# Performance work log

Measured on AMD Instinct MI355X. Metric: run time of the kernel, lower is better.

## Reference

```python
import jax, jax.numpy as jnp
import numpy as np

B, H, W, C = 16, 32, 32, 512
L, CT = 77, 512
NH, HD = 8, 64
G = 32          # GroupNorm groups
EPS = 1e-6      # flax GroupNorm default epsilon
NEG = -1e10


def group_norm(x, scale, bias):
    # flax GroupNorm on [b, n, c]: stats over (n, channels-within-group) per (b, group)
    b, n, c = x.shape
    xg = x.reshape(b, n, G, c // G)
    mu = xg.mean(axis=(1, 3), keepdims=True)
    var = xg.var(axis=(1, 3), keepdims=True)
    xg = (xg - mu) * jax.lax.rsqrt(var + EPS)
    return xg.reshape(b, n, c) * scale + bias


def setup_inputs() -> dict:
    key = jax.random.key(0)
    ks = jax.random.split(key, 8)
    w = lambda k, shape: jax.random.normal(k, shape, jnp.float32) * 0.02
    return {
        "inputs": jax.random.normal(ks[0], (B, H, W, C), jnp.float32),
        "text_enc": jax.random.normal(ks[1], (B, L, CT), jnp.float32),
        "text_mask": jnp.ones((B, L), jnp.int32),
        "gn_q_scale": jnp.ones((C,), jnp.float32),
        "gn_q_bias": jnp.zeros((C,), jnp.float32),
        "gn_kv_scale": jnp.ones((C,), jnp.float32),
        "gn_kv_bias": jnp.zeros((C,), jnp.float32),
        "gn_t_scale": jnp.ones((CT,), jnp.float32),
        "gn_t_bias": jnp.zeros((CT,), jnp.float32),
        "Wq": w(ks[2], (C, NH, HD)),
        "Wk_self": w(ks[3], (C, NH, HD)),
        "Wv_self": w(ks[4], (C, NH, HD)),
        "Wk_cross": w(ks[5], (CT, NH, HD)),
        "Wv_cross": w(ks[6], (CT, NH, HD)),
        "Wout": w(ks[7], (NH, HD, C)),
    }


def reference(inputs, text_enc, text_mask,
              gn_q_scale, gn_q_bias, gn_kv_scale, gn_kv_bias,
              gn_t_scale, gn_t_bias,
              Wq, Wk_self, Wv_self, Wk_cross, Wv_cross, Wout):
    b, h, w, c = inputs.shape
    n = h * w
    x = inputs.reshape(b, n, c)

    x_q = group_norm(x, gn_q_scale, gn_q_bias)
    x_kv = group_norm(x, gn_kv_scale, gn_kv_bias)
    t = group_norm(text_enc, gn_t_scale, gn_t_bias)

    # q/k/v projections; fused: KV = concat(self-KV from image, cross-KV from text)
    scale = jnp.asarray(1.0 / np.sqrt(HD), inputs.dtype)
    q = jnp.einsum('bqc,chd->bqhd', x_q, Wq) * scale  # scale_attn_logits
    k = jnp.concatenate([jnp.einsum('bkc,chd->bkhd', x_kv, Wk_self),
                         jnp.einsum('blc,chd->blhd', t, Wk_cross)], axis=1)
    v = jnp.concatenate([jnp.einsum('bkc,chd->bkhd', x_kv, Wv_self),
                         jnp.einsum('blc,chd->blhd', t, Wv_cross)], axis=1)

    # make_attention_mask(ones[b,n], concat(ones[b,n], text_mask)) -> [b,1,n,n+l];
    # query mask is all ones so only the KV mask matters.
    kv_mask = jnp.concatenate(
        [jnp.ones((b, n), jnp.bool_), text_mask > 0], axis=1)  # [b, n+l]

    logits = jnp.einsum('bqhd,bkhd->bhqk', q, k)  # [b, nh, n, n+l]
    logits = jnp.where(kv_mask[:, None, None, :], logits, jnp.asarray(NEG, logits.dtype))
    probs = jax.nn.softmax(logits, axis=-1)
    attn = jnp.einsum('bhqk,bkhd->bqhd', probs, v)
    out = jnp.einsum('bqhd,hdc->bqc', attn, Wout)
    return out.reshape(b, h, w, c) + inputs
```

## Files before the change

kernel.cpp:

```cpp
#include <hip/hip_runtime.h>
#include <hip/hip_bf16.h>

typedef __hip_bfloat16 bf16;
typedef __attribute__((ext_vector_type(8))) short short8;
typedef __attribute__((ext_vector_type(4))) float f32x4;
typedef __attribute__((ext_vector_type(16))) float f32x16;
#define MFMA16(a, b, c) __builtin_amdgcn_mfma_f32_16x16x32_bf16(a, b, c, 0, 0, 0)
#define MFMA32(a, b, c) __builtin_amdgcn_mfma_f32_32x32x16_bf16(a, b, c, 0, 0, 0)

#define BB   16
#define CCH  512
#define NN   1024
#define LLT  77
#define LPAD 128
#define NHH  8
#define HDD  64
#define GGN  32
#define NKV  1101
#define KVP  1152
#define QSC  0.18033688f

__device__ __forceinline__ unsigned short f2bu(float f){
  bf16 h = __float2bfloat16(f);
  return *reinterpret_cast<unsigned short*>(&h);
}

__device__ __forceinline__ unsigned pk2(float lo, float hi){
  unsigned r;
  asm("v_cvt_pk_bf16_f32 %0, %1, %2" : "=v"(r) : "v"(lo), "v"(hi));
  return r;
}

__device__ __forceinline__ float fexp2(float x){
  float r;
  asm("v_exp_f32 %0, %1" : "=v"(r) : "v"(x));
  return r;
}

__device__ __forceinline__ void pl32swap(unsigned &a, unsigned &b){
  asm("v_permlane32_swap_b32 %0, %1" : "+v"(a), "+v"(b));
}

__device__ __forceinline__ void gload16(const bf16* g, bf16* l){
  __builtin_amdgcn_global_load_lds(
      (const __attribute__((address_space(1))) unsigned int*)g,
      (__attribute__((address_space(3))) unsigned int*)l,
      16, 0, 0);
}

__global__ __launch_bounds__(256) void gn_norm_kernel(
    const float* __restrict__ x, const float* __restrict__ t,
    const float* __restrict__ gqs, const float* __restrict__ gqb,
    const float* __restrict__ gks, const float* __restrict__ gkb,
    const float* __restrict__ gts, const float* __restrict__ gtb,
    const float* __restrict__ W0, const float* __restrict__ W1,
    const float* __restrict__ W2, const float* __restrict__ W3,
    const float* __restrict__ W4, const float* __restrict__ W5,
    bf16* __restrict__ Wt,
    bf16* __restrict__ Xq, bf16* __restrict__ Xkv, bf16* __restrict__ Tn)
{
  __shared__ float sh1[256], sh2[256], mr[2];
  __shared__ alignas(16) float Ws[64][68];
  const int tid = threadIdx.x;
  const int bid = blockIdx.x;

  if (bid < 512){
    const int b = bid >> 5, g = bid & 31;
    const float* xb = x + (size_t)b * NN * CCH + g * 16;
    float s = 0.f, s2 = 0.f;
    for (int i = tid; i < 4096; i += 256){
      const int n = i >> 2, cq = (i & 3) * 4;
      float4 v = *(const float4*)(xb + (size_t)n * CCH + cq);
      s  += v.x + v.y + v.z + v.w;
      s2 += v.x * v.x + v.y * v.y + v.z * v.z + v.w * v.w;
    }
    sh1[tid] = s; sh2[tid] = s2;
    __syncthreads();
    for (int off = 128; off > 0; off >>= 1){
      if (tid < off){ sh1[tid] += sh1[tid + off]; sh2[tid] += sh2[tid + off]; }
      __syncthreads();
    }
    if (tid == 0){
      const float inv = 1.f / 16384.f;
      const float m = sh1[0] * inv;
      mr[0] = m;
      mr[1] = rsqrtf(sh2[0] * inv - m * m + 1e-6f);
    }
    __syncthreads();
    const float m = mr[0], r = mr[1];
    const int ch0 = g * 16;
    for (int i = tid; i < 4096; i += 256){
      const int n = i >> 2, cq = (i & 3) * 4;
      const int ch = ch0 + cq;
      float4 v  = *(const float4*)(xb + (size_t)n * CCH + cq);
      float4 sq = *(const float4*)(gqs + ch), bq = *(const float4*)(gqb + ch);
      float4 sk = *(const float4*)(gks + ch), bk = *(const float4*)(gkb + ch);
      const float n0 = (v.x - m) * r, n1 = (v.y - m) * r;
      const float n2 = (v.z - m) * r, n3 = (v.w - m) * r;
      uint2 oq, ok;
      oq.x = pk2((n0 * sq.x + bq.x) * QSC, (n1 * sq.y + bq.y) * QSC);
      oq.y = pk2((n2 * sq.z + bq.z) * QSC, (n3 * sq.w + bq.w) * QSC);
      ok.x = pk2(n0 * sk.x + bk.x, n1 * sk.y + bk.y);
      ok.y = pk2(n2 * sk.z + bk.z, n3 * sk.w + bk.w);
      const size_t off = ((size_t)b * NN + n) * CCH + ch;
      *(uint2*)(Xq  + off) = oq;
      *(uint2*)(Xkv + off) = ok;
    }
  } else if (bid < 1024){
    const int b = (bid - 512) >> 5, g = (bid - 512) & 31;
    const float* tb = t + (size_t)b * LLT * CCH + g * 16;
    float s = 0.f, s2 = 0.f;
    for (int i = tid; i < 308; i += 256){
      const int l = i >> 2, cq = (i & 3) * 4;
      float4 v = *(const float4*)(tb + (size_t)l * CCH + cq);
      s  += v.x + v.y + v.z + v.w;
      s2 += v.x * v.x + v.y * v.y + v.z * v.z + v.w * v.w;
    }
    sh1[tid] = s; sh2[tid] = s2;
    __syncthreads();
    for (int off = 128; off > 0; off >>= 1){
      if (tid < off){ sh1[tid] += sh1[tid + off]; sh2[tid] += sh2[tid + off]; }
      __syncthreads();
    }
    if (tid == 0){
      const float inv = 1.f / (float)(LLT * 16);
      const float m = sh1[0] * inv;
      mr[0] = m;
      mr[1] = rsqrtf(sh2[0] * inv - m * m + 1e-6f);
    }
    __syncthreads();
    const float m = mr[0], r = mr[1];
    const int ch0 = g * 16;
    for (int i = tid; i < 512; i += 256){
      const int l = i >> 2, cq = (i & 3) * 4;
      const int ch = ch0 + cq;
      uint2 o;
      if (l < LLT){
        float4 v  = *(const float4*)(tb + (size_t)l * CCH + cq);
        float4 sv = *(const float4*)(gts + ch), bv = *(const float4*)(gtb + ch);
        o.x = pk2((v.x - m) * r * sv.x + bv.x, (v.y - m) * r * sv.y + bv.y);
        o.y = pk2((v.z - m) * r * sv.z + bv.z, (v.w - m) * r * sv.w + bv.w);
      } else {
        o.x = 0u; o.y = 0u;
      }
      *(uint2*)(Tn + ((size_t)b * LPAD + l) * CCH + ch) = o;
    }
  } else {
    const int i = bid - 1024;
    const int wsel = i >> 6;
    const int rem  = i & 63;
    const int n0 = (rem & 7) * 64, k0 = (rem >> 3) * 64;
    const float* W = wsel == 0 ? W0 : wsel == 1 ? W1 : wsel == 2 ? W2 :
                     wsel == 3 ? W3 : wsel == 4 ? W4 : W5;
    bf16* dst = Wt + (size_t)wsel * CCH * CCH;

    const int rr = tid >> 2, c = (tid & 3) * 16;
    const float* src = W + (size_t)(k0 + rr) * CCH + n0 + c;
    *(float4*)&Ws[rr][c]      = *(const float4*)(src);
    *(float4*)&Ws[rr][c + 4]  = *(const float4*)(src + 4);
    *(float4*)&Ws[rr][c + 8]  = *(const float4*)(src + 8);
    *(float4*)&Ws[rr][c + 12] = *(const float4*)(src + 12);
    __syncthreads();

    const int nr = tid >> 2, kc = (tid & 3) * 16;
    uint4 o0, o1;
    o0.x = pk2(Ws[kc + 0][nr],  Ws[kc + 1][nr]);
    o0.y = pk2(Ws[kc + 2][nr],  Ws[kc + 3][nr]);
    o0.z = pk2(Ws[kc + 4][nr],  Ws[kc + 5][nr]);
    o0.w = pk2(Ws[kc + 6][nr],  Ws[kc + 7][nr]);
    o1.x = pk2(Ws[kc + 8][nr],  Ws[kc + 9][nr]);
    o1.y = pk2(Ws[kc + 10][nr], Ws[kc + 11][nr]);
    o1.z = pk2(Ws[kc + 12][nr], Ws[kc + 13][nr]);
    o1.w = pk2(Ws[kc + 14][nr], Ws[kc + 15][nr]);
    bf16* d = dst + (size_t)(n0 + nr) * CCH + k0 + kc;
    *(uint4*)d = o0;
    *(uint4*)(d + 8) = o1;
  }
}

__global__ __launch_bounds__(256) void proj_all_mfma(
    const bf16* __restrict__ Xq, const bf16* __restrict__ Xkv,
    const bf16* __restrict__ Tn, const bf16* __restrict__ Wt,
    bf16* __restrict__ Qo, bf16* __restrict__ Ko, bf16* __restrict__ Vo)
{
  __shared__ alignas(16) char SHRAW[65536];
  const int tid  = threadIdx.x;
  const int wave = tid >> 6, lane = tid & 63;
  const int l16 = lane & 15, quad = lane >> 4;
  const int bx = blockIdx.x;

  if (bx < 1536){
    bf16 (*T)[4][64][64] = reinterpret_cast<bf16(*)[4][64][64]>(SHRAW);
    const int wr = wave >> 1, wc = wave & 1;
    const int ct = bx >> 7;
    const int rt = bx & 127;
    const int mat = ct >> 2;
    const int cm0 = (ct & 3) * 128;
    const int b  = rt >> 3;
    const int n0 = (rt & 7) * 128;

    const bf16* A  = (mat == 0) ? Xq : Xkv;
    const bf16* Bw = Wt + (size_t)mat * CCH * CCH + (size_t)cm0 * CCH;

    f32x4 acc[4][4];
    #pragma unroll
    for (int rf = 0; rf < 4; rf++)
      #pragma unroll
      for (int cf = 0; cf < 4; cf++) acc[rf][cf] = (f32x4){0.f,0.f,0.f,0.f};

    const int lrow = lane >> 3, lcol = (lane & 7) * 8;
    const bf16* srcbase = (wave < 2)
        ? A  + ((size_t)b * NN + n0 + wave * 64) * CCH
        : Bw + (size_t)((wave - 2) * 64) * CCH;

    #pragma unroll
    for (int c = 0; c < 8; c++)
      gload16(srcbase + (size_t)(c * 8 + lrow) * CCH + lcol, &T[0][wave][c * 8][0]);
    __syncthreads();

    int cur = 0;
    for (int kt = 0; kt < 8; kt++){
      if (kt < 7){
        const int kc = (kt + 1) * 64;
        #pragma unroll
        for (int c = 0; c < 8; c++)
          gload16(srcbase + (size_t)(c * 8 + lrow) * CCH + kc + lcol,
                  &T[cur ^ 1][wave][c * 8][0]);
      }

      short8 af[4][2];
      #pragma unroll
      for (int rf = 0; rf < 4; rf++){
        af[rf][0] = *(const short8*)&T[cur][wr][rf * 16 + l16][quad * 8];
        af[rf][1] = *(const short8*)&T[cur][wr][rf * 16 + l16][32 + quad * 8];
      }
      #pragma unroll
      for (int cf = 0; cf < 4; cf++){
        const short8 b0 = *(const short8*)&T[cur][2 + wc][cf * 16 + l16][quad * 8];
        const short8 b1 = *(const short8*)&T[cur][2 + wc][cf * 16 + l16][32 + quad * 8];
        #pragma unroll
        for (int rf = 0; rf < 4; rf++){
          acc[rf][cf] = MFMA16(af[rf][0], b0, acc[rf][cf]);
          acc[rf][cf] = MFMA16(af[rf][1], b1, acc[rf][cf]);
        }
      }
      __syncthreads();
      cur ^= 1;
    }

    const int h  = (cm0 + wc * 64) >> 6;
    const int nb = n0 + wr * 64;
    bf16 (*Tw)[64] = reinterpret_cast<bf16(*)[64]>(SHRAW + wave * 8192);

    if (mat < 2){
      bf16* Out = (mat == 0) ? Qo : Ko;
      const int stride = (mat == 0) ? NN : KVP;
      #pragma unroll
      for (int rf = 0; rf < 4; rf++)
        #pragma unroll
        for (int cf = 0; cf < 4; cf++)
          #pragma unroll
          for (int r = 0; r < 4; r++)
            Tw[rf * 16 + quad * 4 + r][cf * 16 + l16] =
                __float2bfloat16(acc[rf][cf][r]);
      const int rr = lane >> 2, cs = (lane & 3) * 16;
      #pragma unroll
      for (int k2 = 0; k2 < 4; k2++){
        const int row = rr + k2 * 16;
        bf16* od = Out + (((size_t)b * NHH + h) * stride + nb + row) * HDD + cs;
        *(uint4*)od       = *(const uint4*)&Tw[row][cs];
        *(uint4*)(od + 8) = *(const uint4*)&Tw[row][cs + 8];
      }
    } else {
      #pragma unroll
      for (int cf = 0; cf < 4; cf++)
        #pragma unroll
        for (int rf = 0; rf < 4; rf++)
          #pragma unroll
          for (int r = 0; r < 4; r++)
            Tw[cf * 16 + l16][rf * 16 + quad * 4 + r] =
                __float2bfloat16(acc[rf][cf][r]);
      __syncthreads();
      const int dl = lane >> 2, cseg = (lane & 3) * 16;
      #pragma unroll
      for (int k2 = 0; k2 < 4; k2++){
        const int d = dl + k2 * 16;
        bf16* vd = Vo + (((size_t)b * NHH + h) * HDD + d) * KVP + nb + cseg;
        *(uint4*)vd       = *(const uint4*)&Tw[d][cseg];
        *(uint4*)(vd + 8) = *(const uint4*)&Tw[d][cseg + 8];
      }
    }
  } else {
    bf16 (*At)[72] = reinterpret_cast<bf16(*)[72]>(SHRAW);
    bf16 (*Bk)[72] = reinterpret_cast<bf16(*)[72]>(SHRAW + 64 * 72 * 2);
    bf16 (*Bv)[72] = reinterpret_cast<bf16(*)[72]>(SHRAW + 2 * 64 * 72 * 2);
    const int i  = bx - 1536;
    const int h  = i & 7;
    const int l0 = ((i >> 3) & 1) * 64;
    const int b  = i >> 4;

    const bf16* Wkc = Wt + 3 * (size_t)CCH * CCH;
    const bf16* Wvc = Wt + 4 * (size_t)CCH * CCH;

    f32x4 sk[4], sv[4];
    #pragma unroll
    for (int nt = 0; nt < 4; nt++){
      sk[nt] = (f32x4){0.f,0.f,0.f,0.f};
      sv[nt] = (f32x4){0.f,0.f,0.f,0.f};
    }

    const int sr = tid >> 2, sc = (tid & 3) * 16;
    const bf16* p_a  = Tn  + ((size_t)b * LPAD + l0 + sr) * CCH + sc;
    const bf16* p_bk = Wkc + (size_t)(h * 64 + sr) * CCH + sc;
    const bf16* p_bv = Wvc + (size_t)(h * 64 + sr) * CCH + sc;

    uint4 ra0 = *(const uint4*)p_a,   ra1 = *(const uint4*)(p_a + 8);
    uint4 rk0 = *(const uint4*)p_bk,  rk1 = *(const uint4*)(p_bk + 8);
    uint4 rv0 = *(const uint4*)p_bv,  rv1 = *(const uint4*)(p_bv + 8);

    for (int kt = 0; kt < 8; kt++){
      *(uint4*)&At[sr][sc]     = ra0;  *(uint4*)&At[sr][sc + 8] = ra1;
      *(uint4*)&Bk[sr][sc]     = rk0;  *(uint4*)&Bk[sr][sc + 8] = rk1;
      *(uint4*)&Bv[sr][sc]     = rv0;  *(uint4*)&Bv[sr][sc + 8] = rv1;
      if (kt < 7){
        const int k1 = (kt + 1) * 64;
        ra0 = *(const uint4*)(p_a + k1);   ra1 = *(const uint4*)(p_a + k1 + 8);
        rk0 = *(const uint4*)(p_bk + k1);  rk1 = *(const uint4*)(p_bk + k1 + 8);
        rv0 = *(const uint4*)(p_bv + k1);  rv1 = *(const uint4*)(p_bv + k1 + 8);
      }
      __syncthreads();

      const short8 a0 = *(const short8*)&At[wave * 16 + l16][quad * 8];
      const short8 a1 = *(const short8*)&At[wave * 16 + l16][32 + quad * 8];
      #pragma unroll
      for (int nt = 0; nt < 4; nt++){
        const short8 bk0 = *(const short8*)&Bk[nt * 16 + l16][quad * 8];
        const short8 bk1 = *(const short8*)&Bk[nt * 16 + l16][32 + quad * 8];
        sk[nt] = MFMA16(a0, bk0, sk[nt]);
        sk[nt] = MFMA16(a1, bk1, sk[nt]);
        const short8 bv0 = *(const short8*)&Bv[nt * 16 + l16][quad * 8];
        const short8 bv1 = *(const short8*)&Bv[nt * 16 + l16][32 + quad * 8];
        sv[nt] = MFMA16(a0, bv0, sv[nt]);
        sv[nt] = MFMA16(a1, bv1, sv[nt]);
      }
      __syncthreads();
    }

    #pragma unroll
    for (int r = 0; r < 4; r++){
      int kvrow = NN + l0 + wave * 16 + quad * 4 + r;
      bf16* kd = Ko + (((size_t)b * NHH + h) * KVP + kvrow) * HDD + l16;
      #pragma unroll
      for (int nt = 0; nt < 4; nt++)
        kd[nt * 16] = __float2bfloat16(sk[nt][r]);
    }

    __syncthreads();
    #pragma unroll
    for (int nt = 0; nt < 4; nt++)
      #pragma unroll
      for (int r = 0; r < 4; r++)
        Bk[nt * 16 + l16][wave * 16 + quad * 4 + r] = __float2bfloat16(sv[nt][r]);
    __syncthreads();
    {
      int d = tid >> 2, c = (tid & 3) * 16;
      bf16* vd = Vo + (((size_t)b * NHH + h) * HDD + d) * KVP + NN + l0 + c;
      *(uint4*)vd       = *(const uint4*)&Bk[d][c];
      *(uint4*)(vd + 8) = *(const uint4*)&Bk[d][c + 8];
    }
  }
}

__global__ __launch_bounds__(256, 4) void attn_mfma_kernel(
    const bf16* __restrict__ Q, const bf16* __restrict__ K,
    const bf16* __restrict__ Vt, const int* __restrict__ tmask,
    bf16* __restrict__ Ao)
{
  const int tid  = threadIdx.x;
  const int wave = tid >> 6;
  const int lane = tid & 63;
  const int l31  = lane & 31;
  const int hi   = lane >> 5;
  const int bx = blockIdx.x;
  const int q0 = (bx >> 7) * 128;
  const int g  = bx & 127;
  const int h  = g & 7;
  const int b  = g >> 3;

  __shared__ alignas(16) bf16 KV[2][2][64][72];

  const bf16* qp = Q + (((size_t)b * NHH + h) * NN + q0 + wave * 32 + l31) * HDD + hi * 8;
  short8 qf[4];
  qf[0] = *(const short8*)(qp);
  qf[1] = *(const short8*)(qp + 16);
  qf[2] = *(const short8*)(qp + 32);
  qf[3] = *(const short8*)(qp + 48);

  union { unsigned u[4]; short8 s8; } ones;
  ones.u[0] = 0x3F803F80u; ones.u[1] = 0x3F803F80u;
  ones.u[2] = 0x3F803F80u; ones.u[3] = 0x3F803F80u;

  f32x16 zf;
  #pragma unroll
  for (int i = 0; i < 16; i++) zf[i] = 0.f;

  f32x16 o_acc[2], l_acc;
  #pragma unroll
  for (int dt = 0; dt < 2; dt++)
    #pragma unroll
    for (int i = 0; i < 16; i++) o_acc[dt][i] = 0.f;
  #pragma unroll
  for (int i = 0; i < 16; i++) l_acc[i] = 0.f;

  const size_t kbase = ((size_t)b * NHH + h) * KVP;
  const size_t vbase = ((size_t)b * NHH + h) * (size_t)HDD * KVP;

  const int sr = tid >> 2;
  const int sc = (tid & 3) * 16;
  const bf16* kp = K  + (kbase + sr) * HDD + sc;
  const bf16* vp = Vt + vbase + (size_t)sr * KVP + sc;

  uint4 kr0 = *(const uint4*)kp, kr1 = *(const uint4*)(kp + 8);
  uint4 vr0 = *(const uint4*)vp, vr1 = *(const uint4*)(vp + 8);
  *(uint4*)&KV[0][0][sr][sc]     = kr0;
  *(uint4*)&KV[0][0][sr][sc + 8] = kr1;
  *(uint4*)&KV[0][1][sr][sc]     = vr0;
  *(uint4*)&KV[0][1][sr][sc + 8] = vr1;
  kr0 = *(const uint4*)(kp + 4096); kr1 = *(const uint4*)(kp + 4096 + 8);
  vr0 = *(const uint4*)(vp + 64);   vr1 = *(const uint4*)(vp + 64 + 8);
  __syncthreads();

  for (int kt = 0; kt < 18; kt++){
    const int cur = kt & 1;
    if (kt + 1 < 18){
      *(uint4*)&KV[cur ^ 1][0][sr][sc]     = kr0;
      *(uint4*)&KV[cur ^ 1][0][sr][sc + 8] = kr1;
      *(uint4*)&KV[cur ^ 1][1][sr][sc]     = vr0;
      *(uint4*)&KV[cur ^ 1][1][sr][sc + 8] = vr1;
    }
    if (kt + 2 < 18){
      const size_t ko = (size_t)(kt + 2) * 4096;
      const int    vo = (kt + 2) * 64;
      kr0 = *(const uint4*)(kp + ko); kr1 = *(const uint4*)(kp + ko + 8);
      vr0 = *(const uint4*)(vp + vo); vr1 = *(const uint4*)(vp + vo + 8);
    }

    const bf16 (*Ks)[72] = KV[cur][0];
    const bf16 (*Vs)[72] = KV[cur][1];
    const int kv0 = kt * 64;

    #pragma unroll
    for (int t = 0; t < 2; t++){
      const short8 kf0 = *(const short8*)&Ks[t * 32 + l31][hi * 8];
      const short8 kf1 = *(const short8*)&Ks[t * 32 + l31][16 + hi * 8];
      const short8 kf2 = *(const short8*)&Ks[t * 32 + l31][32 + hi * 8];
      const short8 kf3 = *(const short8*)&Ks[t * 32 + l31][48 + hi * 8];
      __builtin_amdgcn_s_setprio(1);
      f32x16 s = MFMA32(kf0, qf[0], zf);
      s = MFMA32(kf1, qf[1], s);
      s = MFMA32(kf2, qf[2], s);
      s = MFMA32(kf3, qf[3], s);
      __builtin_amdgcn_s_setprio(0);

      if (kv0 + 64 > NN){
        #pragma unroll
        for (int r = 0; r < 16; r++){
          int idx = kv0 - NN + t * 32 + (r & 3) + 8 * (r >> 2) + 4 * hi;
          int ci = idx < LLT ? idx : LLT - 1;
          float rep = (idx < LLT)
                        ? (tmask[b * LLT + ci] > 0 ? 1e30f : -1e10f)
                        : -1e30f;
          s[r] = fminf(s[r], rep);
        }
      }

      #pragma unroll
      for (int r = 0; r < 16; r++) s[r] = fexp2(s[r]);

      unsigned w0 = pk2(s[0],  s[1]),  w1 = pk2(s[2],  s[3]);
      unsigned w2 = pk2(s[4],  s[5]),  w3 = pk2(s[6],  s[7]);
      unsigned w4 = pk2(s[8],  s[9]),  w5 = pk2(s[10], s[11]);
      unsigned w6 = pk2(s[12], s[13]), w7 = pk2(s[14], s[15]);
      pl32swap(w0, w2);
      pl32swap(w1, w3);
      pl32swap(w4, w6);
      pl32swap(w5, w7);
      union { unsigned u[4]; short8 s8; } pf0, pf1;
      pf0.u[0] = w0; pf0.u[1] = w1; pf0.u[2] = w2; pf0.u[3] = w3;
      pf1.u[0] = w4; pf1.u[1] = w5; pf1.u[2] = w6; pf1.u[3] = w7;

      const short8 vf00 = *(const short8*)&Vs[l31][t * 32 + hi * 8];
      const short8 vf01 = *(const short8*)&Vs[l31][t * 32 + 16 + hi * 8];
      const short8 vf10 = *(const short8*)&Vs[32 + l31][t * 32 + hi * 8];
      const short8 vf11 = *(const short8*)&Vs[32 + l31][t * 32 + 16 + hi * 8];

      __builtin_amdgcn_s_setprio(1);
      l_acc = MFMA32(pf0.s8, ones.s8, l_acc);
      l_acc = MFMA32(pf1.s8, ones.s8, l_acc);
      o_acc[0] = MFMA32(pf0.s8, vf00, o_acc[0]);
      o_acc[0] = MFMA32(pf1.s8, vf01, o_acc[0]);
      o_acc[1] = MFMA32(pf0.s8, vf10, o_acc[1]);
      o_acc[1] = MFMA32(pf1.s8, vf11, o_acc[1]);
      __builtin_amdgcn_s_setprio(0);
    }
    __syncthreads();
  }

  #pragma unroll
  for (int r = 0; r < 16; r++){
    const int ql = (r & 3) + 8 * (r >> 2) + 4 * hi;
    const float linv = 1.f / l_acc[r];
    const int n = q0 + wave * 32 + ql;
    bf16* dst = Ao + ((size_t)b * NN + n) * CCH + h * HDD + l31;
    dst[0]  = __float2bfloat16(o_acc[0][r] * linv);
    dst[32] = __float2bfloat16(o_acc[1][r] * linv);
  }
}

__global__ __launch_bounds__(256) void outproj_mfma(
    const bf16* __restrict__ A, const bf16* __restrict__ Wt,
    const float* __restrict__ resid, float* __restrict__ out)
{
  __shared__ alignas(16) char SH[36864];
  bf16 (*T)[64][64] = reinterpret_cast<bf16(*)[64][64]>(SH);
  const int tid  = threadIdx.x;
  const int wave = tid >> 6, lane = tid & 63;
  const int l16 = lane & 15, quad = lane >> 4;
  const int wr = wave >> 1, wc = wave & 1;
  const int bx = blockIdx.x;
  const int c0 = (bx >> 7) * 128;
  const int g0 = (bx & 127) * 128;

  const bf16* Bw = Wt + (size_t)5 * CCH * CCH + (size_t)c0 * CCH;

  f32x4 acc[4][4];
  #pragma unroll
  for (int rf = 0; rf < 4; rf++)
    #pragma unroll
    for (int cf = 0; cf < 4; cf++) acc[rf][cf] = (f32x4){0.f,0.f,0.f,0.f};

  const int lrow = lane >> 3, lcol = (lane & 7) * 8;
  const bf16* srcbase = (wave < 2)
      ? A  + ((size_t)g0 + wave * 64) * CCH
      : Bw + (size_t)((wave - 2) * 64) * CCH;

  for (int kt = 0; kt < 8; kt++){
    const int kc = kt * 64;
    #pragma unroll
    for (int c = 0; c < 8; c++){
      const bf16* g = srcbase + (size_t)(c * 8 + lrow) * CCH + kc + lcol;
      gload16(g, &T[wave][c * 8][0]);
    }
    __syncthreads();

    short8 af[4][2];
    #pragma unroll
    for (int rf = 0; rf < 4; rf++){
      af[rf][0] = *(const short8*)&T[wr][rf * 16 + l16][quad * 8];
      af[rf][1] = *(const short8*)&T[wr][rf * 16 + l16][32 + quad * 8];
    }
    #pragma unroll
    for (int cf = 0; cf < 4; cf++){
      const short8 b0 = *(const short8*)&T[2 + wc][cf * 16 + l16][quad * 8];
      const short8 b1 = *(const short8*)&T[2 + wc][cf * 16 + l16][32 + quad * 8];
      #pragma unroll
      for (int rf = 0; rf < 4; rf++){
        acc[rf][cf] = MFMA16(af[rf][0], b0, acc[rf][cf]);
        acc[rf][cf] = MFMA16(af[rf][1], b1, acc[rf][cf]);
      }
    }
    __syncthreads();
  }

  float (*Tf)[68] = reinterpret_cast<float(*)[68]>(SH + wave * 8704);
  const int cg = (lane & 15) * 4;
  #pragma unroll
  for (int hf = 0; hf < 2; hf++){
    #pragma unroll
    for (int rf = 0; rf < 2; rf++)
      #pragma unroll
      for (int cf = 0; cf < 4; cf++)
        #pragma unroll
        for (int r = 0; r < 4; r++)
          Tf[rf * 16 + quad * 4 + r][cf * 16 + l16] = acc[hf * 2 + rf][cf][r];
    #pragma unroll
    for (int k = 0; k < 8; k++){
      const int row32 = k * 4 + quad;
      const size_t grow = (size_t)g0 + wr * 64 + hf * 32 + row32;
      const int gcol = c0 + wc * 64 + cg;
      float4 v  = *(const float4*)&Tf[row32][cg];
      float4 rz = *(const float4*)&resid[grow * CCH + gcol];
      v.x += rz.x; v.y += rz.y; v.z += rz.z; v.w += rz.w;
      *(float4*)&out[grow * CCH + gcol] = v;
    }
    if (hf == 0){
      asm volatile("s_waitcnt lgkmcnt(0)" ::: "memory");
      __builtin_amdgcn_sched_barrier(0);
    }
  }
}

extern "C" void kernel_launch(void* const* d_in, const int* in_sizes, int n_in,
                              void* d_out, int out_size, void* d_ws, size_t ws_size,
                              hipStream_t stream)
{
  const float* x     = (const float*)d_in[0];
  const float* txt   = (const float*)d_in[1];
  const int*   tmask = (const int*)d_in[2];
  const float* gqs   = (const float*)d_in[3];
  const float* gqb   = (const float*)d_in[4];
  const float* gks   = (const float*)d_in[5];
  const float* gkb   = (const float*)d_in[6];
  const float* gts   = (const float*)d_in[7];
  const float* gtb   = (const float*)d_in[8];
  const float* Wq    = (const float*)d_in[9];
  const float* Wks   = (const float*)d_in[10];
  const float* Wvs   = (const float*)d_in[11];
  const float* Wkc   = (const float*)d_in[12];
  const float* Wvc   = (const float*)d_in[13];
  const float* Wout  = (const float*)d_in[14];

  float* stats = (float*)d_ws;
  bf16* WtAll = (bf16*)(stats + 2048);
  bf16* Xq  = WtAll + (size_t)6 * CCH * CCH;
  bf16* Xkv = Xq  + (size_t)BB * NN * CCH;
  bf16* Tn  = Xkv + (size_t)BB * NN * CCH;
  bf16* Qw  = Tn  + (size_t)BB * LPAD * CCH;
  bf16* Kw  = Qw  + (size_t)BB * NHH * NN * HDD;
  bf16* Vw  = Kw  + (size_t)BB * NHH * KVP * HDD;
  bf16* Aw  = Xq;

  gn_norm_kernel<<<1408, 256, 0, stream>>>(
      x, txt, gqs, gqb, gks, gkb, gts, gtb,
      Wq, Wks, Wvs, Wkc, Wvc, Wout, WtAll, Xq, Xkv, Tn);
  proj_all_mfma<<<1792, 256, 0, stream>>>(
      Xq, Xkv, Tn, WtAll, Qw, Kw, Vw);
  attn_mfma_kernel<<<1024, 256, 0, stream>>>(Qw, Kw, Vw, tmask, Aw);
  outproj_mfma<<<512, 256, 0, stream>>>(Aw, WtAll, x, (float*)d_out);
}
```

Before: 259.6 us.

## Fuse GroupNorm apply into projection GEMM A-tile staging via per-channel affine coefficients

The GroupNorm kernel now emits only per-(batch, channel) scale and shift coefficients instead of writing normalized bf16 copies of the image for Q and KV. The projection GEMM reads fp32 x directly, applies the affine transform in registers and writes swizzled bf16 into LDS. The global loads for the next tile are issued before the MFMAs and the conversion happens after them. This removes a large bf16 write and re-read of two normalized activation tensors. In exchange, x is read in fp32 once per column tile, so more global traffic goes into the GEMM, and there is extra VALU work plus register pressure.

New measurement: 254.7 us. Within noise of the previous version (-1.9%).

```diff
diff --git a/kernel.cpp b/kernel.cpp
--- a/kernel.cpp
+++ b/kernel.cpp
@@ -48,7 +48,7 @@
       16, 0, 0);
 }
 
-__global__ __launch_bounds__(256) void gn_norm_kernel(
+__global__ __launch_bounds__(256) void pre_kernel(
     const float* __restrict__ x, const float* __restrict__ t,
     const float* __restrict__ gqs, const float* __restrict__ gqb,
     const float* __restrict__ gks, const float* __restrict__ gkb,
@@ -57,7 +57,9 @@
     const float* __restrict__ W2, const float* __restrict__ W3,
     const float* __restrict__ W4, const float* __restrict__ W5,
     bf16* __restrict__ Wt,
-    bf16* __restrict__ Xq, bf16* __restrict__ Xkv, bf16* __restrict__ Tn)
+    float* __restrict__ cAq, float* __restrict__ cBq,
+    float* __restrict__ cAk, float* __restrict__ cBk,
+    bf16* __restrict__ Tn)
 {
   __shared__ float sh1[256], sh2[256], mr[2];
   __shared__ alignas(16) float Ws[64][68];
@@ -87,24 +89,15 @@
       mr[1] = rsqrtf(sh2[0] * inv - m * m + 1e-6f);
     }
     __syncthreads();
-    const float m = mr[0], r = mr[1];
-    const int ch0 = g * 16;
-    for (int i = tid; i < 4096; i += 256){
-      const int n = i >> 2, cq = (i & 3) * 4;
-      const int ch = ch0 + cq;
-      float4 v  = *(const float4*)(xb + (size_t)n * CCH + cq);
-      float4 sq = *(const float4*)(gqs + ch), bq = *(const float4*)(gqb + ch);
-      float4 sk = *(const float4*)(gks + ch), bk = *(const float4*)(gkb + ch);
-      const float n0 = (v.x - m) * r, n1 = (v.y - m) * r;
-      const float n2 = (v.z - m) * r, n3 = (v.w - m) * r;
-      uint2 oq, ok;
-      oq.x = pk2((n0 * sq.x + bq.x) * QSC, (n1 * sq.y + bq.y) * QSC);
-      oq.y = pk2((n2 * sq.z + bq.z) * QSC, (n3 * sq.w + bq.w) * QSC);
-      ok.x = pk2(n0 * sk.x + bk.x, n1 * sk.y + bk.y);
-      ok.y = pk2(n2 * sk.z + bk.z, n3 * sk.w + bk.w);
-      const size_t off = ((size_t)b * NN + n) * CCH + ch;
-      *(uint2*)(Xq  + off) = oq;
-      *(uint2*)(Xkv + off) = ok;
+    if (tid < 16){
+      const int ch = g * 16 + tid;
+      const float m = mr[0], r = mr[1];
+      const float aq = r * gqs[ch] * QSC;
+      cAq[b * CCH + ch] = aq;
+      cBq[b * CCH + ch] = gqb[ch] * QSC - m * aq;
+      const float ak = r * gks[ch];
+      cAk[b * CCH + ch] = ak;
+      cBk[b * CCH + ch] = gkb[ch] - m * ak;
     }
   } else if (bid < 1024){
     const int b = (bid - 512) >> 5, g = (bid - 512) & 31;
@@ -179,7 +172,9 @@
 }
 
 __global__ __launch_bounds__(256) void proj_all_mfma(
-    const bf16* __restrict__ Xq, const bf16* __restrict__ Xkv,
+    const float* __restrict__ x,
+    const float* __restrict__ cAq, const float* __restrict__ cBq,
+    const float* __restrict__ cAk, const float* __restrict__ cBk,
     const bf16* __restrict__ Tn, const bf16* __restrict__ Wt,
     bf16* __restrict__ Qo, bf16* __restrict__ Ko, bf16* __restrict__ Vo)
 {
@@ -199,8 +194,10 @@
     const int b  = rt >> 3;
     const int n0 = (rt & 7) * 128;
 
-    const bf16* A  = (mat == 0) ? Xq : Xkv;
-    const bf16* Bw = Wt + (size_t)mat * CCH * CCH + (size_t)cm0 * CCH;
+    const bf16*  Bw   = Wt + (size_t)mat * CCH * CCH + (size_t)cm0 * CCH;
+    const float* xsrc = x + ((size_t)b * NN + n0) * CCH;
+    const float* cA   = (mat == 0) ? cAq : cAk;
+    const float* cB   = (mat == 0) ? cBq : cBk;
 
     f32x4 acc[4][4];
     #pragma unroll
@@ -208,31 +205,71 @@
       #pragma unroll
       for (int cf = 0; cf < 4; cf++) acc[rf][cf] = (f32x4){0.f,0.f,0.f,0.f};
 
+    const int sr = tid >> 2, sc4 = (tid & 3) * 16;
+    const int c0ch = sc4 >> 3;
     const int lrow = lane >> 3, lcol = (lane & 7) * 8;
-    const bf16* srcbase = (wave < 2)
-        ? A  + ((size_t)b * NN + n0 + wave * 64) * CCH
-        : Bw + (size_t)((wave - 2) * 64) * CCH;
-
-    #pragma unroll
-    for (int c = 0; c < 8; c++)
-      gload16(srcbase + (size_t)(c * 8 + lrow) * CCH + lcol, &T[0][wave][c * 8][0]);
+    const bf16* bsrc = Bw + (size_t)(((wave - 2) & 3) * 64) * CCH;
+
+    float4 av[2][4];
+    auto earlyA = [&](int kc){
+      const float* s0 = xsrc + (size_t)sr * CCH + kc + sc4;
+      const float* s1 = s0 + (size_t)64 * CCH;
+      av[0][0] = *(const float4*)s0;       av[0][1] = *(const float4*)(s0 + 4);
+      av[0][2] = *(const float4*)(s0 + 8); av[0][3] = *(const float4*)(s0 + 12);
+      av[1][0] = *(const float4*)s1;       av[1][1] = *(const float4*)(s1 + 4);
+      av[1][2] = *(const float4*)(s1 + 8); av[1][3] = *(const float4*)(s1 + 12);
+    };
+    auto lateA = [&](int kc, int buf){
+      const int ch = kc + sc4;
+      const float* pa = cA + b * CCH + ch;
+      const float* pb = cB + b * CCH + ch;
+      const float4 a0 = *(const float4*)pa,       a1 = *(const float4*)(pa + 4);
+      const float4 a2 = *(const float4*)(pa + 8), a3 = *(const float4*)(pa + 12);
+      const float4 b0 = *(const float4*)pb,       b1 = *(const float4*)(pb + 4);
+      const float4 b2 = *(const float4*)(pb + 8), b3 = *(const float4*)(pb + 12);
+      #pragma unroll
+      for (int a = 0; a < 2; a++){
+        uint4 w0, w1;
+        w0.x = pk2(av[a][0].x * a0.x + b0.x, av[a][0].y * a0.y + b0.y);
+        w0.y = pk2(av[a][0].z * a0.z + b0.z, av[a][0].w * a0.w + b0.w);
+        w0.z = pk2(av[a][1].x * a1.x + b1.x, av[a][1].y * a1.y + b1.y);
+        w0.w = pk2(av[a][1].z * a1.z + b1.z, av[a][1].w * a1.w + b1.w);
+        w1.x = pk2(av[a][2].x * a2.x + b2.x, av[a][2].y * a2.y + b2.y);
+        w1.y = pk2(av[a][2].z * a2.z + b2.z, av[a][2].w * a2.w + b2.w);
+        w1.z = pk2(av[a][3].x * a3.x + b3.x, av[a][3].y * a3.y + b3.y);
+        w1.w = pk2(av[a][3].z * a3.z + b3.z, av[a][3].w * a3.w + b3.w);
+        bf16* base = &T[buf][a][sr][0];
+        *(uint4*)(base + ((( c0ch     ) ^ (sr & 7)) << 3)) = w0;
+        *(uint4*)(base + (((c0ch + 1) ^ (sr & 7)) << 3)) = w1;
+      }
+    };
+    auto stageB = [&](int kc, int buf){
+      if (wave >= 2){
+        #pragma unroll
+        for (int c = 0; c < 8; c++)
+          gload16(bsrc + (size_t)(c * 8 + lrow) * CCH + kc + lcol,
+                  &T[buf][wave][c * 8][0]);
+      }
+    };
+
+    stageB(0, 0);
+    earlyA(0);
+    lateA(0, 0);
     __syncthreads();
 
     int cur = 0;
     for (int kt = 0; kt < 8; kt++){
       if (kt < 7){
-        const int kc = (kt + 1) * 64;
-        #pragma unroll
-        for (int c = 0; c < 8; c++)
-          gload16(srcbase + (size_t)(c * 8 + lrow) * CCH + kc + lcol,
-                  &T[cur ^ 1][wave][c * 8][0]);
+        stageB((kt + 1) * 64, cur ^ 1);
+        earlyA((kt + 1) * 64);
       }
 
       short8 af[4][2];
       #pragma unroll
       for (int rf = 0; rf < 4; rf++){
-        af[rf][0] = *(const short8*)&T[cur][wr][rf * 16 + l16][quad * 8];
-        af[rf][1] = *(const short8*)&T[cur][wr][rf * 16 + l16][32 + quad * 8];
+        const int rr = rf * 16 + l16;
+        af[rf][0] = *(const short8*)&T[cur][wr][rr][((quad    ) ^ (rr & 7)) << 3];
+        af[rf][1] = *(const short8*)&T[cur][wr][rr][((quad + 4) ^ (rr & 7)) << 3];
       }
       #pragma unroll
       for (int cf = 0; cf < 4; cf++){
@@ -244,6 +281,8 @@
           acc[rf][cf] = MFMA16(af[rf][1], b1, acc[rf][cf]);
         }
       }
+
+      if (kt < 7) lateA((kt + 1) * 64, cur ^ 1);
       __syncthreads();
       cur ^= 1;
     }
@@ -630,11 +669,17 @@
   bf16* Vw  = Kw  + (size_t)BB * NHH * KVP * HDD;
   bf16* Aw  = Xq;
 
-  gn_norm_kernel<<<1408, 256, 0, stream>>>(
+  float* cAq = (float*)Xkv;
+  float* cBq = cAq + BB * CCH;
+  float* cAk = cBq + BB * CCH;
+  float* cBk = cAk + BB * CCH;
+
+  pre_kernel<<<1408, 256, 0, stream>>>(
       x, txt, gqs, gqb, gks, gkb, gts, gtb,
-      Wq, Wks, Wvs, Wkc, Wvc, Wout, WtAll, Xq, Xkv, Tn);
+      Wq, Wks, Wvs, Wkc, Wvc, Wout, WtAll,
+      cAq, cBq, cAk, cBk, Tn);
   proj_all_mfma<<<1792, 256, 0, stream>>>(
-      Xq, Xkv, Tn, WtAll, Qw, Kw, Vw);
+      x, cAq, cBq, cAk, cBk, Tn, WtAll, Qw, Kw, Vw);
   attn_mfma_kernel<<<1024, 256, 0, stream>>>(Qw, Kw, Vw, tmask, Aw);
   outproj_mfma<<<512, 256, 0, stream>>>(Aw, WtAll, x, (float*)d_out);
 }
```
